# Kernel tuning notes

Measured on AMD Instinct MI355X. Metric: run time of the kernel, lower is better.

The kernel has to match this reference:

```python
import jax, jax.numpy as jnp
import numpy as np

N = 50000       # nodes
E = 800000      # edges (before self-loops)
F_IN = 128
HID = 64
HEADS = 4
OUT_DIM = 128
N_CLS = 2
NG = 500        # num graphs
SLOPE = 0.2     # GATConv leaky_relu negative slope
EPS = 1e-5      # BatchNorm eps


def setup_inputs() -> dict:
    key = jax.random.key(0)
    ks = jax.random.split(key, 24)
    s = 0.05
    d = {
        "x": jax.random.normal(ks[0], (N, F_IN), jnp.float32),
        "edge_index": jax.random.randint(ks[1], (2, E), 0, N, jnp.int64),
        "batch": jnp.sort(jax.random.randint(ks[2], (N,), 0, NG, jnp.int64)),
        # GATConv 1
        "W1": jax.random.normal(ks[3], (F_IN, HEADS * HID), jnp.float32) * s,
        "att_src1": jax.random.normal(ks[4], (HEADS, HID), jnp.float32) * s,
        "att_dst1": jax.random.normal(ks[5], (HEADS, HID), jnp.float32) * s,
        "b1": jnp.zeros((HEADS * HID,), jnp.float32),
        # BN1 (eval mode)
        "g1": jnp.ones((HEADS * HID,), jnp.float32),
        "be1": jnp.zeros((HEADS * HID,), jnp.float32),
        "rm1": jnp.zeros((HEADS * HID,), jnp.float32),
        "rv1": jnp.ones((HEADS * HID,), jnp.float32),
        # GATConv 2
        "W2": jax.random.normal(ks[6], (HEADS * HID, HEADS * HID), jnp.float32) * s,
        "att_src2": jax.random.normal(ks[7], (HEADS, HID), jnp.float32) * s,
        "att_dst2": jax.random.normal(ks[8], (HEADS, HID), jnp.float32) * s,
        "b2": jnp.zeros((HEADS * HID,), jnp.float32),
        # BN2 (eval mode)
        "g2": jnp.ones((HEADS * HID,), jnp.float32),
        "be2": jnp.zeros((HEADS * HID,), jnp.float32),
        "rm2": jnp.zeros((HEADS * HID,), jnp.float32),
        "rv2": jnp.ones((HEADS * HID,), jnp.float32),
        # MLP head
        "lw1": jax.random.normal(ks[9], (HEADS * HID, OUT_DIM), jnp.float32) * s,
        "lb1": jnp.zeros((OUT_DIM,), jnp.float32),
        "lw2": jax.random.normal(ks[10], (OUT_DIM, N_CLS), jnp.float32) * s,
        "lb2": jnp.zeros((N_CLS,), jnp.float32),
    }
    return d


def _gat_conv(x, src, dst, W, a_src, a_dst, b):
    """PyG GATConv (concat heads, add_self_loops=True, eval -> no dropout)."""
    n = x.shape[0]
    h = (x @ W).reshape(n, HEADS, -1)            # [N, H, C]
    loop = jnp.arange(n)
    s = jnp.concatenate([src, loop])             # self-loops appended
    d = jnp.concatenate([dst, loop])
    a_s = jnp.sum(h * a_src, axis=-1)            # [N, H]
    a_d = jnp.sum(h * a_dst, axis=-1)            # [N, H]
    e = jax.nn.leaky_relu(a_s[s] + a_d[d], SLOPE)   # [Et, H]
    # softmax over incoming edges per destination node
    m = jax.ops.segment_max(e, d, num_segments=n)
    ex = jnp.exp(e - m[d])
    denom = jax.ops.segment_sum(ex, d, num_segments=n)
    alpha = ex / denom[d]                        # [Et, H]
    msg = h[s] * alpha[:, :, None]               # [Et, H, C]
    out = jax.ops.segment_sum(msg, d, num_segments=n)
    return out.reshape(n, -1) + b


def _bn_eval(x, g, be, rm, rv):
    return (x - rm) * jax.lax.rsqrt(rv + EPS) * g + be


def reference(x, edge_index, batch, W1, att_src1, att_dst1, b1, g1, be1, rm1, rv1,
              W2, att_src2, att_dst2, b2, g2, be2, rm2, rv2, lw1, lb1, lw2, lb2):
    src, dst = edge_index[0], edge_index[1]
    h = jax.nn.relu(_gat_conv(x, src, dst, W1, att_src1, att_dst1, b1))
    h = _bn_eval(h, g1, be1, rm1, rv1)
    h = jax.nn.relu(_gat_conv(h, src, dst, W2, att_src2, att_dst2, b2))
    h = _bn_eval(h, g2, be2, rm2, rv2)
    # global mean pool over graphs
    sums = jax.ops.segment_sum(h, batch, num_segments=NG)
    cnt = jax.ops.segment_sum(jnp.ones((h.shape[0],), h.dtype), batch, num_segments=NG)
    pooled = sums / jnp.clip(cnt, 1.0)[:, None]
    z = jax.nn.relu(pooled @ lw1 + lb1)
    return z @ lw2 + lb2
```

## Files before the change

### kernel.cpp

```cpp
#include <hip/hip_runtime.h>
#include <hip/hip_bf16.h>
#include <math.h>

#define N_NODES 50000
#define M_PAD   50048
#define TILE_M  64
#define NBLK_GEMM (M_PAD / TILE_M)
#define N_EDGES 800000
#define EHALF   (N_EDGES / 2)
#define NBLK_BUILD ((EHALF + 255) / 256)
#define F_IN 128
#define HID 64
#define HEADS 4
#define FEAT 256
#define OUT_DIM 128
#define N_CLS 2
#define NG 500
#define SLOPE 0.2f
#define BN_EPS 1e-5f
#define ECAP 64

#define XCONV (N_NODES * F_IN / 8)
#define T_W1  (F_IN * 256)
#define T_W2  (FEAT * 256)
#define XPAD_ULL ((M_PAD - N_NODES) * F_IN / 4)
#define HPAD_ULL ((M_PAD - N_NODES) * FEAT / 4)
#define PREP_THREADS (XCONV + T_W1 + T_W2 + XPAD_ULL + HPAD_ULL + N_NODES)
#define NBLK_PREP ((PREP_THREADS + 255) / 256)

typedef __attribute__((ext_vector_type(8))) short short8;
typedef __attribute__((ext_vector_type(4))) float floatx4;
typedef __attribute__((ext_vector_type(2))) float floatx2;

__device__ inline unsigned short f2bf(float f) {
    unsigned int u = __float_as_uint(f);
    unsigned int lsb = (u >> 16) & 1u;
    return (unsigned short)((u + 0x7fffu + lsb) >> 16);
}

__global__ __launch_bounds__(256) void prep(
    const float* __restrict__ x, const float* __restrict__ W1,
    const float* __restrict__ W2,
    unsigned short* __restrict__ xbf, unsigned short* __restrict__ W1T,
    unsigned short* __restrict__ W2T, unsigned short* __restrict__ h1bf,
    int* __restrict__ deg, unsigned short* __restrict__ ell,
    int* __restrict__ ovf_cnt) {
    int gid = blockIdx.x * 256 + threadIdx.x;
    if (gid < XCONV) {
        const float4* xp = (const float4*)&x[gid * 8];
        float4 f0 = xp[0], f1 = xp[1];
        uint4 pk;
        pk.x = (unsigned)f2bf(f0.x) | ((unsigned)f2bf(f0.y) << 16);
        pk.y = (unsigned)f2bf(f0.z) | ((unsigned)f2bf(f0.w) << 16);
        pk.z = (unsigned)f2bf(f1.x) | ((unsigned)f2bf(f1.y) << 16);
        pk.w = (unsigned)f2bf(f1.z) | ((unsigned)f2bf(f1.w) << 16);
        *(uint4*)&xbf[gid * 8] = pk;
        return;
    }
    int j = gid - XCONV;
    if (j < T_W1) {
        int k = j >> 8, n = j & 255;
        W1T[n * F_IN + k] = f2bf(W1[j]);
        return;
    }
    j -= T_W1;
    if (j < T_W2) {
        int k = j >> 8, n = j & 255;
        W2T[n * FEAT + k] = f2bf(W2[j]);
        return;
    }
    j -= T_W2;
    if (j < XPAD_ULL) {
        ((unsigned long long*)(xbf + (size_t)N_NODES * F_IN))[j] = 0ULL;
        return;
    }
    j -= XPAD_ULL;
    if (j < HPAD_ULL) {
        ((unsigned long long*)(h1bf + (size_t)N_NODES * FEAT))[j] = 0ULL;
        return;
    }
    j -= HPAD_ULL;
    if (j < N_NODES) {
        deg[j] = 1;
        ell[(size_t)j * ECAP] = (unsigned short)j;
        if (j == 0) *ovf_cnt = 0;
    }
}

template<int K, bool BUILD>
__global__ __launch_bounds__(256, 4) void gemm_mfma(
    const unsigned short* __restrict__ Ab, const unsigned short* __restrict__ BT,
    const float* __restrict__ att_src, const float* __restrict__ att_dst,
    unsigned char* __restrict__ h8, float* __restrict__ a_s,
    float* __restrict__ a_d,
    const int* __restrict__ src, const int* __restrict__ dst,
    int* __restrict__ deg, unsigned short* __restrict__ ell,
    int* __restrict__ ovf_cnt, int* __restrict__ ovf) {
    constexpr int LS = 40;
    constexpr int C8 = 272;
    __shared__ __align__(16) unsigned char smem_raw[(TILE_M + FEAT) * LS * 2];
    int t = threadIdx.x;

    if (BUILD && blockIdx.x < NBLK_BUILD) {
        int i = blockIdx.x * 256 + t;
        if (i >= EHALF) return;
        int s0 = src[i],          d0 = dst[i];
        int s1 = src[i + EHALF],  d1 = dst[i + EHALF];
        int p0 = atomicAdd(&deg[d0], 1);
        int p1 = atomicAdd(&deg[d1], 1);
        if (p0 < ECAP) {
            ell[(size_t)d0 * ECAP + p0] = (unsigned short)s0;
        } else {
            int k = atomicAdd(ovf_cnt, 1);
            ovf[2 * k] = s0; ovf[2 * k + 1] = d0;
        }
        if (p1 < ECAP) {
            ell[(size_t)d1 * ECAP + p1] = (unsigned short)s1;
        } else {
            int k = atomicAdd(ovf_cnt, 1);
            ovf[2 * k] = s1; ovf[2 * k + 1] = d1;
        }
        return;
    }

    int bid = BUILD ? (int)blockIdx.x - NBLK_BUILD : (int)blockIdx.x;
    unsigned short* As = (unsigned short*)smem_raw;
    unsigned short* Bs = As + TILE_M * LS;
    unsigned char*  s8 = smem_raw;
    int lane = t & 63, w = t >> 6;
    int row0 = bid * TILE_M;
    int mrow = lane & 15, quad = lane >> 4;

    floatx4 acc[4][4] = {};

    int rA = t >> 2, cA = (t & 3) * 8;

    for (int k0 = 0; k0 < K; k0 += 32) {
        *(uint4*)&As[rA * LS + cA] =
            *(const uint4*)&Ab[(long long)(row0 + rA) * K + k0 + cA];
        #pragma unroll
        for (int j = 0; j < 4; j++) {
            int r = rA + j * 64;
            *(uint4*)&Bs[r * LS + cA] = *(const uint4*)&BT[(long long)r * K + k0 + cA];
        }
        __syncthreads();
        short8 bf[4];
        #pragma unroll
        for (int ni = 0; ni < 4; ni++)
            bf[ni] = *(const short8*)&Bs[(w * 64 + ni * 16 + mrow) * LS + quad * 8];
        #pragma unroll
        for (int mi = 0; mi < 4; mi++) {
            short8 af = *(const short8*)&As[(mi * 16 + mrow) * LS + quad * 8];
            #pragma unroll
            for (int ni = 0; ni < 4; ni++)
                acc[mi][ni] = __builtin_amdgcn_mfma_f32_16x16x32_bf16(af, bf[ni],
                                                                      acc[mi][ni], 0, 0, 0);
        }
        __syncthreads();
    }

    float ats[4], atd[4];
    #pragma unroll
    for (int ni = 0; ni < 4; ni++) {
        ats[ni] = att_src[w * 64 + ni * 16 + mrow];
        atd[ni] = att_dst[w * 64 + ni * 16 + mrow];
    }
    #pragma unroll
    for (int mi = 0; mi < 4; mi++) {
        #pragma unroll
        for (int r = 0; r < 4; r++) {
            int row = row0 + mi * 16 + quad * 4 + r;
            float ps = 0.f, pd = 0.f;
            #pragma unroll
            for (int ni = 0; ni < 4; ni++) {
                float v = acc[mi][ni][r];
                ps += v * ats[ni];
                pd += v * atd[ni];
            }
            #pragma unroll
            for (int off = 1; off < 16; off <<= 1) {
                ps += __shfl_xor(ps, off);
                pd += __shfl_xor(pd, off);
            }
            if (mrow == 0 && row < N_NODES) {
                a_s[row * 4 + w] = ps;
                a_d[row * 4 + w] = pd;
            }
        }
    }

    #pragma unroll
    for (int mi = 0; mi < 4; mi++)
        #pragma unroll
        for (int r = 0; r < 4; r++) {
            int row = mi * 16 + quad * 4 + r;
            #pragma unroll
            for (int ni = 0; ni < 4; ni += 2) {
                int pk = __builtin_amdgcn_cvt_pk_fp8_f32(acc[mi][ni][r],
                                                         acc[mi][ni + 1][r], 0, false);
                s8[row * C8 + w * 64 + ni * 16 + mrow]       = (unsigned char)(pk & 0xff);
                s8[row * C8 + w * 64 + (ni + 1) * 16 + mrow] = (unsigned char)((pk >> 8) & 0xff);
            }
        }
    __syncthreads();
    {
        int r2 = t >> 2, q = t & 3;
        const uint4* sp = (const uint4*)&s8[r2 * C8 + q * 64];
        uint4* dp = (uint4*)&h8[(long long)(row0 + r2) * FEAT + q * 64];
        #pragma unroll
        for (int k = 0; k < 4; k++)
            dp[k] = sp[k];
    }
}

__global__ __launch_bounds__(256) void gat_fused(
    const int* __restrict__ deg_arr, const unsigned short* __restrict__ ell,
    const int* __restrict__ ovf_cnt, const int* __restrict__ ovf,
    const float* __restrict__ a_s, const float* __restrict__ a_d,
    const unsigned char* __restrict__ h8, const float* __restrict__ bias,
    const float* __restrict__ g, const float* __restrict__ be,
    const float* __restrict__ rm, const float* __restrict__ rv,
    unsigned short* __restrict__ out16) {
    int t = threadIdx.x;
    int lane = t & 63;
    int w = t >> 6;
    int hd = lane >> 4;
    int d = blockIdx.x * 4 + w;

    __shared__ float p_lds[4 * ECAP * 4];
    __shared__ int   o_lds[4 * ECAP];
    float* pw = &p_lds[w * ECAP * 4];
    int*   ow = &o_lds[w * ECAP];

    const unsigned int* __restrict__ H1 = (const unsigned int*)h8;

    int deg = deg_arr[d];
    float4 ad4 = *(const float4*)&a_d[d * 4];

    float den = 0.f;
    float4 acc = make_float4(0.f, 0.f, 0.f, 0.f);

    if (deg <= ECAP) {
        float lg[4] = {-INFINITY, -INFINITY, -INFINITY, -INFINITY};
        if (lane < deg) {
            int s = ell[(size_t)d * ECAP + lane];
            ow[lane] = s * 64;
            float4 as4 = *(const float4*)&a_s[s * 4];
            float e0 = as4.x + ad4.x; lg[0] = e0 > 0.f ? e0 : SLOPE * e0;
            float e1 = as4.y + ad4.y; lg[1] = e1 > 0.f ? e1 : SLOPE * e1;
            float e2 = as4.z + ad4.z; lg[2] = e2 > 0.f ? e2 : SLOPE * e2;
            float e3 = as4.w + ad4.w; lg[3] = e3 > 0.f ? e3 : SLOPE * e3;
        }
        float mm = fmaxf(fmaxf(lg[0], lg[1]), fmaxf(lg[2], lg[3]));
        #pragma unroll
        for (int off = 1; off < 64; off <<= 1) mm = fmaxf(mm, __shfl_xor(mm, off));
        if (lane < deg) {
            float4 pq;
            pq.x = __expf(lg[0] - mm);
            pq.y = __expf(lg[1] - mm);
            pq.z = __expf(lg[2] - mm);
            pq.w = __expf(lg[3] - mm);
            *(float4*)&pw[lane * 4] = pq;
        }
        int e = 0;
        for (; e + 1 < deg; e += 2) {
            int oA = ow[e], oB = ow[e + 1];
            float pA = pw[e * 4 + hd], pB = pw[(e + 1) * 4 + hd];
            int uA = (int)H1[oA + lane];
            int uB = (int)H1[oB + lane];
            den += pA + pB;
            floatx2 a0 = __builtin_amdgcn_cvt_pk_f32_fp8(uA, false);
            floatx2 a1 = __builtin_amdgcn_cvt_pk_f32_fp8(uA, true);
            floatx2 b0 = __builtin_amdgcn_cvt_pk_f32_fp8(uB, false);
            floatx2 b1 = __builtin_amdgcn_cvt_pk_f32_fp8(uB, true);
            acc.x += pA * a0.x; acc.y += pA * a0.y;
            acc.z += pA * a1.x; acc.w += pA * a1.y;
            acc.x += pB * b0.x; acc.y += pB * b0.y;
            acc.z += pB * b1.x; acc.w += pB * b1.y;
        }
        if (e < deg) {
            int oA = ow[e];
            float pA = pw[e * 4 + hd];
            int uA = (int)H1[oA + lane];
            den += pA;
            floatx2 a0 = __builtin_amdgcn_cvt_pk_f32_fp8(uA, false);
            floatx2 a1 = __builtin_amdgcn_cvt_pk_f32_fp8(uA, true);
            acc.x += pA * a0.x; acc.y += pA * a0.y;
            acc.z += pA * a1.x; acc.w += pA * a1.y;
        }
    } else {
        float m_old;
        {
            int s = ell[(size_t)d * ECAP + lane];
            ow[lane] = s * 64;
            float4 as4 = *(const float4*)&a_s[s * 4];
            float lg[4];
            float e0 = as4.x + ad4.x; lg[0] = e0 > 0.f ? e0 : SLOPE * e0;
            float e1 = as4.y + ad4.y; lg[1] = e1 > 0.f ? e1 : SLOPE * e1;
            float e2 = as4.z + ad4.z; lg[2] = e2 > 0.f ? e2 : SLOPE * e2;
            float e3 = as4.w + ad4.w; lg[3] = e3 > 0.f ? e3 : SLOPE * e3;
            float mm = fmaxf(fmaxf(lg[0], lg[1]), fmaxf(lg[2], lg[3]));
            #pragma unroll
            for (int off = 1; off < 64; off <<= 1) mm = fmaxf(mm, __shfl_xor(mm, off));
            m_old = mm;
            float4 pq;
            pq.x = __expf(lg[0] - mm);
            pq.y = __expf(lg[1] - mm);
            pq.z = __expf(lg[2] - mm);
            pq.w = __expf(lg[3] - mm);
            *(float4*)&pw[lane * 4] = pq;
            for (int e = 0; e < ECAP; e++) {
                int oA = ow[e];
                float pA = pw[e * 4 + hd];
                int uA = (int)H1[oA + lane];
                den += pA;
                floatx2 a0 = __builtin_amdgcn_cvt_pk_f32_fp8(uA, false);
                floatx2 a1 = __builtin_amdgcn_cvt_pk_f32_fp8(uA, true);
                acc.x += pA * a0.x; acc.y += pA * a0.y;
                acc.z += pA * a1.x; acc.w += pA * a1.y;
            }
        }
        int nov = *ovf_cnt;
        for (int i = 0; i < nov; i++) {
            int s2 = ovf[2 * i], d2 = ovf[2 * i + 1];
            if (d2 != d) continue;
            float4 as4 = *(const float4*)&a_s[s2 * 4];
            float lg[4];
            float e0 = as4.x + ad4.x; lg[0] = e0 > 0.f ? e0 : SLOPE * e0;
            float e1 = as4.y + ad4.y; lg[1] = e1 > 0.f ? e1 : SLOPE * e1;
            float e2 = as4.z + ad4.z; lg[2] = e2 > 0.f ? e2 : SLOPE * e2;
            float e3 = as4.w + ad4.w; lg[3] = e3 > 0.f ? e3 : SLOPE * e3;
            float mmax = fmaxf(fmaxf(lg[0], lg[1]), fmaxf(lg[2], lg[3]));
            float m_new = fmaxf(m_old, mmax);
            float alpha = __expf(m_old - m_new);
            m_old = m_new;
            float ph = __expf(lg[hd] - m_new);
            acc.x *= alpha; acc.y *= alpha; acc.z *= alpha; acc.w *= alpha;
            den = den * alpha + ph;
            int u = (int)H1[s2 * 64 + lane];
            floatx2 a0 = __builtin_amdgcn_cvt_pk_f32_fp8(u, false);
            floatx2 a1 = __builtin_amdgcn_cvt_pk_f32_fp8(u, true);
            acc.x += ph * a0.x; acc.y += ph * a0.y;
            acc.z += ph * a1.x; acc.w += ph * a1.y;
        }
    }
    float inv = 1.f / den;
    int c0 = lane * 4;
    float4 bi = *(const float4*)&bias[c0];
    float4 gg = *(const float4*)&g[c0];
    float4 bb = *(const float4*)&be[c0];
    float4 mm4 = *(const float4*)&rm[c0];
    float4 vv = *(const float4*)&rv[c0];
    float v0 = fmaxf(acc.x * inv + bi.x, 0.f);
    float v1 = fmaxf(acc.y * inv + bi.y, 0.f);
    float v2 = fmaxf(acc.z * inv + bi.z, 0.f);
    float v3 = fmaxf(acc.w * inv + bi.w, 0.f);
    v0 = (v0 - mm4.x) * rsqrtf(vv.x + BN_EPS) * gg.x + bb.x;
    v1 = (v1 - mm4.y) * rsqrtf(vv.y + BN_EPS) * gg.y + bb.y;
    v2 = (v2 - mm4.z) * rsqrtf(vv.z + BN_EPS) * gg.z + bb.z;
    v3 = (v3 - mm4.w) * rsqrtf(vv.w + BN_EPS) * gg.w + bb.w;
    unsigned long long o =
        (unsigned long long)f2bf(v0) |
        ((unsigned long long)f2bf(v1) << 16) |
        ((unsigned long long)f2bf(v2) << 32) |
        ((unsigned long long)f2bf(v3) << 48);
    __builtin_nontemporal_store(o, (unsigned long long*)&out16[(long long)d * FEAT + c0]);
}

__global__ __launch_bounds__(256) void head_fused(
    const unsigned short* __restrict__ h2, const int* __restrict__ batch,
    const float* __restrict__ lw1, const float* __restrict__ lb1,
    const float* __restrict__ lw2, const float* __restrict__ lb2,
    float* __restrict__ out) {
    int gph = blockIdx.x;
    int t = threadIdx.x;
    __shared__ float pooled[FEAT];
    __shared__ float zl[OUT_DIM];
    __shared__ int lo_s, hi_s;
    if (t == 0) {
        int lo = 0, hi = N_NODES;
        while (lo < hi) { int mid = (lo + hi) >> 1; if (batch[mid] < gph) lo = mid + 1; else hi = mid; }
        lo_s = lo;
        int lo2 = 0, hi2 = N_NODES;
        while (lo2 < hi2) { int mid = (lo2 + hi2) >> 1; if (batch[mid] < gph + 1) lo2 = mid + 1; else hi2 = mid; }
        hi_s = lo2;
    }
    __syncthreads();
    int lo = lo_s, hi = hi_s;
    float a0 = 0.f, a1 = 0.f, a2 = 0.f, a3 = 0.f;
    int n = lo;
    for (; n + 3 < hi; n += 4) {
        a0 += __uint_as_float((unsigned)h2[(long long)n * FEAT + t] << 16);
        a1 += __uint_as_float((unsigned)h2[(long long)(n + 1) * FEAT + t] << 16);
        a2 += __uint_as_float((unsigned)h2[(long long)(n + 2) * FEAT + t] << 16);
        a3 += __uint_as_float((unsigned)h2[(long long)(n + 3) * FEAT + t] << 16);
    }
    for (; n < hi; n++) a0 += __uint_as_float((unsigned)h2[(long long)n * FEAT + t] << 16);
    float cnt = fmaxf((float)(hi - lo), 1.f);
    pooled[t] = (a0 + a1 + a2 + a3) / cnt;
    __syncthreads();
    int j = t >> 1, kh = t & 1;
    float zp = 0.f;
    #pragma unroll 8
    for (int k = kh * 128; k < kh * 128 + 128; k++)
        zp += pooled[k] * lw1[k * OUT_DIM + j];
    zp += __shfl_xor(zp, 1);
    if (kh == 0) zl[j] = fmaxf(zp + lb1[j], 0.f);
    __syncthreads();
    int w = t >> 6, lane = t & 63;
    if (w < 2) {
        float p = zl[lane] * lw2[lane * 2 + w] + zl[lane + 64] * lw2[(lane + 64) * 2 + w];
        #pragma unroll
        for (int off = 1; off < 64; off <<= 1) p += __shfl_xor(p, off);
        if (lane == 0) out[gph * 2 + w] = p + lb2[w];
    }
}

extern "C" void kernel_launch(void* const* d_in, const int* in_sizes, int n_in,
                              void* d_out, int out_size, void* d_ws, size_t ws_size,
                              hipStream_t stream) {
    const float* x       = (const float*)d_in[0];
    const int*   ei      = (const int*)d_in[1];
    const int*   batch   = (const int*)d_in[2];
    const float* W1      = (const float*)d_in[3];
    const float* att_s1  = (const float*)d_in[4];
    const float* att_d1  = (const float*)d_in[5];
    const float* b1      = (const float*)d_in[6];
    const float* g1      = (const float*)d_in[7];
    const float* be1     = (const float*)d_in[8];
    const float* rm1     = (const float*)d_in[9];
    const float* rv1     = (const float*)d_in[10];
    const float* W2      = (const float*)d_in[11];
    const float* att_s2  = (const float*)d_in[12];
    const float* att_d2  = (const float*)d_in[13];
    const float* b2      = (const float*)d_in[14];
    const float* g2      = (const float*)d_in[15];
    const float* be2     = (const float*)d_in[16];
    const float* rm2     = (const float*)d_in[17];
    const float* rv2     = (const float*)d_in[18];
    const float* lw1     = (const float*)d_in[19];
    const float* lb1     = (const float*)d_in[20];
    const float* lw2     = (const float*)d_in[21];
    const float* lb2     = (const float*)d_in[22];
    float* out           = (float*)d_out;

    const int* src = ei;
    const int* dst = ei + N_EDGES;

    char* p = (char*)d_ws;
    auto carve = [&p](size_t bytes) -> void* {
        void* r = (void*)p;
        p += (bytes + 63) & ~(size_t)63;
        return r;
    };
    unsigned short* h2bf = (unsigned short*)carve(sizeof(short) * (size_t)N_NODES * FEAT);
    float* a_s    = (float*)carve(sizeof(float) * N_NODES * HEADS);
    float* a_d    = (float*)carve(sizeof(float) * N_NODES * HEADS);
    int*   deg    = (int*)carve(sizeof(int) * N_NODES);
    int*   ovf_cnt= (int*)carve(sizeof(int) * 16);
    unsigned short* ell = (unsigned short*)carve(sizeof(short) * (size_t)N_NODES * ECAP);
    int*   ovf    = (int*)carve(sizeof(int) * 2 * (N_EDGES + N_NODES));
    unsigned char*  h8   = (unsigned char*)carve((size_t)M_PAD * FEAT);
    unsigned short* xbf  = (unsigned short*)carve(sizeof(short) * (size_t)M_PAD * F_IN);
    unsigned short* h1bf = (unsigned short*)carve(sizeof(short) * (size_t)M_PAD * FEAT);
    unsigned short* w1t  = (unsigned short*)carve(sizeof(short) * FEAT * F_IN);
    unsigned short* w2t  = (unsigned short*)carve(sizeof(short) * FEAT * FEAT);

    prep<<<NBLK_PREP, 256, 0, stream>>>(
        x, W1, W2, xbf, w1t, w2t, h1bf, deg, ell, ovf_cnt);

    gemm_mfma<F_IN, true><<<NBLK_BUILD + NBLK_GEMM, 256, 0, stream>>>(
        xbf, w1t, att_s1, att_d1, h8, a_s, a_d,
        src, dst, deg, ell, ovf_cnt, ovf);
    gat_fused<<<N_NODES / 4, 256, 0, stream>>>(deg, ell, ovf_cnt, ovf, a_s, a_d, h8,
                                               b1, g1, be1, rm1, rv1, h1bf);

    gemm_mfma<FEAT, false><<<NBLK_GEMM, 256, 0, stream>>>(
        h1bf, w2t, att_s2, att_d2, h8, a_s, a_d,
        nullptr, nullptr, nullptr, nullptr, nullptr, nullptr);
    gat_fused<<<N_NODES / 4, 256, 0, stream>>>(deg, ell, ovf_cnt, ovf, a_s, a_d, h8,
                                               b2, g2, be2, rm2, rv2, h2bf);

    head_fused<<<NG, 256, 0, stream>>>(h2bf, batch, lw1, lb1, lw2, lb2, out);
}
```

Before: 309.9 us.

## Fuse x bf16 conversion into GEMM1 and software-pipeline GAT neighbor gathers

Drops the separate x-to-bf16 conversion pass in prep and converts fp32 x to bf16 while loading the A tile inside the first GEMM, which saves a full write and reread of the converted input. GEMM blocks are now placed before the edge-build blocks in the combined launch. The GAT aggregation loop is rewritten to gather four neighbor rows per step, with the next group prefetched (zero-padded to a multiple of four), so more loads are in flight. The ELL neighbor list widens from 16-bit to 32-bit indices, which doubles its memory traffic.

```diff
diff --git a/kernel.cpp b/kernel.cpp
--- a/kernel.cpp
+++ b/kernel.cpp
@@ -20,12 +20,10 @@
 #define BN_EPS 1e-5f
 #define ECAP 64
 
-#define XCONV (N_NODES * F_IN / 8)
 #define T_W1  (F_IN * 256)
 #define T_W2  (FEAT * 256)
-#define XPAD_ULL ((M_PAD - N_NODES) * F_IN / 4)
 #define HPAD_ULL ((M_PAD - N_NODES) * FEAT / 4)
-#define PREP_THREADS (XCONV + T_W1 + T_W2 + XPAD_ULL + HPAD_ULL + N_NODES)
+#define PREP_THREADS (T_W1 + T_W2 + HPAD_ULL + N_NODES)
 #define NBLK_PREP ((PREP_THREADS + 255) / 256)
 
 typedef __attribute__((ext_vector_type(8))) short short8;
@@ -38,43 +36,24 @@
     return (unsigned short)((u + 0x7fffu + lsb) >> 16);
 }
 
-__global__ __launch_bounds__(256) void prep(
-    const float* __restrict__ x, const float* __restrict__ W1,
-    const float* __restrict__ W2,
-    unsigned short* __restrict__ xbf, unsigned short* __restrict__ W1T,
-    unsigned short* __restrict__ W2T, unsigned short* __restrict__ h1bf,
-    int* __restrict__ deg, unsigned short* __restrict__ ell,
-    int* __restrict__ ovf_cnt) {
+__global__ __launch_bounds__(256) void prep_small(
+    const float* __restrict__ W1, const float* __restrict__ W2,
+    unsigned short* __restrict__ W1T, unsigned short* __restrict__ W2T,
+    unsigned short* __restrict__ h1bf,
+    int* __restrict__ deg, int* __restrict__ ell, int* __restrict__ ovf_cnt) {
     int gid = blockIdx.x * 256 + threadIdx.x;
-    if (gid < XCONV) {
-        const float4* xp = (const float4*)&x[gid * 8];
-        float4 f0 = xp[0], f1 = xp[1];
-        uint4 pk;
-        pk.x = (unsigned)f2bf(f0.x) | ((unsigned)f2bf(f0.y) << 16);
-        pk.y = (unsigned)f2bf(f0.z) | ((unsigned)f2bf(f0.w) << 16);
-        pk.z = (unsigned)f2bf(f1.x) | ((unsigned)f2bf(f1.y) << 16);
-        pk.w = (unsigned)f2bf(f1.z) | ((unsigned)f2bf(f1.w) << 16);
-        *(uint4*)&xbf[gid * 8] = pk;
+    if (gid < T_W1) {
+        int k = gid >> 8, n = gid & 255;
+        W1T[n * F_IN + k] = f2bf(W1[gid]);
         return;
     }
-    int j = gid - XCONV;
-    if (j < T_W1) {
-        int k = j >> 8, n = j & 255;
-        W1T[n * F_IN + k] = f2bf(W1[j]);
-        return;
-    }
-    j -= T_W1;
+    int j = gid - T_W1;
     if (j < T_W2) {
         int k = j >> 8, n = j & 255;
         W2T[n * FEAT + k] = f2bf(W2[j]);
         return;
     }
     j -= T_W2;
-    if (j < XPAD_ULL) {
-        ((unsigned long long*)(xbf + (size_t)N_NODES * F_IN))[j] = 0ULL;
-        return;
-    }
-    j -= XPAD_ULL;
     if (j < HPAD_ULL) {
         ((unsigned long long*)(h1bf + (size_t)N_NODES * FEAT))[j] = 0ULL;
         return;
@@ -82,139 +61,171 @@
     j -= HPAD_ULL;
     if (j < N_NODES) {
         deg[j] = 1;
-        ell[(size_t)j * ECAP] = (unsigned short)j;
+        ell[(size_t)j * ECAP] = j;
         if (j == 0) *ovf_cnt = 0;
     }
 }
 
-template<int K, bool BUILD>
-__global__ __launch_bounds__(256, 4) void gemm_mfma(
-    const unsigned short* __restrict__ Ab, const unsigned short* __restrict__ BT,
+template<int K, bool AF32>
+__device__ __forceinline__ void gemm_core(
+    const void* __restrict__ Av, const unsigned short* __restrict__ BT,
+    const float* __restrict__ att_src, const float* __restrict__ att_dst,
+    unsigned char* __restrict__ h8, float* __restrict__ a_s,
+    float* __restrict__ a_d, int bid, unsigned char* smem_raw) {
+    constexpr int LS = 40;
+    constexpr int C8 = 272;
+    int t = threadIdx.x;
+    unsigned short* As = (unsigned short*)smem_raw;
+    unsigned short* Bs = As + TILE_M * LS;
+    unsigned char*  s8 = smem_raw;
+    int lane = t & 63, w = t >> 6;
+    int row0 = bid * TILE_M;
+    int mrow = lane & 15, quad = lane >> 4;
+
+    floatx4 acc[4][4] = {};
+
+    int rA = t >> 2, cA = (t & 3) * 8;
+
+    const unsigned short* Ab = (const unsigned short*)Av;
+    const float* Af = (const float*)Av;
+
+    for (int k0 = 0; k0 < K; k0 += 32) {
+        if (AF32) {
+            uint4 pk = make_uint4(0, 0, 0, 0);
+            if (row0 + rA < N_NODES) {
+                float4 f0 = *(const float4*)&Af[(long long)(row0 + rA) * K + k0 + cA];
+                float4 f1 = *(const float4*)&Af[(long long)(row0 + rA) * K + k0 + cA + 4];
+                pk.x = (unsigned)f2bf(f0.x) | ((unsigned)f2bf(f0.y) << 16);
+                pk.y = (unsigned)f2bf(f0.z) | ((unsigned)f2bf(f0.w) << 16);
+                pk.z = (unsigned)f2bf(f1.x) | ((unsigned)f2bf(f1.y) << 16);
+                pk.w = (unsigned)f2bf(f1.z) | ((unsigned)f2bf(f1.w) << 16);
+            }
+            *(uint4*)&As[rA * LS + cA] = pk;
+        } else {
+            *(uint4*)&As[rA * LS + cA] =
+                *(const uint4*)&Ab[(long long)(row0 + rA) * K + k0 + cA];
+        }
+        #pragma unroll
+        for (int j = 0; j < 4; j++) {
+            int r = rA + j * 64;
+            *(uint4*)&Bs[r * LS + cA] = *(const uint4*)&BT[(long long)r * K + k0 + cA];
+        }
+        __syncthreads();
+        short8 bf[4];
+        #pragma unroll
+        for (int ni = 0; ni < 4; ni++)
+            bf[ni] = *(const short8*)&Bs[(w * 64 + ni * 16 + mrow) * LS + quad * 8];
+        #pragma unroll
+        for (int mi = 0; mi < 4; mi++) {
+            short8 af = *(const short8*)&As[(mi * 16 + mrow) * LS + quad * 8];
+            #pragma unroll
+            for (int ni = 0; ni < 4; ni++)
+                acc[mi][ni] = __builtin_amdgcn_mfma_f32_16x16x32_bf16(af, bf[ni],
+                                                                      acc[mi][ni], 0, 0, 0);
+        }
+        __syncthreads();
+    }
+
+    float ats[4], atd[4];
+    #pragma unroll
+    for (int ni = 0; ni < 4; ni++) {
+        ats[ni] = att_src[w * 64 + ni * 16 + mrow];
+        atd[ni] = att_dst[w * 64 + ni * 16 + mrow];
+    }
+    #pragma unroll
+    for (int mi = 0; mi < 4; mi++) {
+        #pragma unroll
+        for (int r = 0; r < 4; r++) {
+            int row = row0 + mi * 16 + quad * 4 + r;
+            float ps = 0.f, pd = 0.f;
+            #pragma unroll
+            for (int ni = 0; ni < 4; ni++) {
+                float v = acc[mi][ni][r];
+                ps += v * ats[ni];
+                pd += v * atd[ni];
+            }
+            #pragma unroll
+            for (int off = 1; off < 16; off <<= 1) {
+                ps += __shfl_xor(ps, off);
+                pd += __shfl_xor(pd, off);
+            }
+            if (mrow == 0 && row < N_NODES) {
+                a_s[row * 4 + w] = ps;
+                a_d[row * 4 + w] = pd;
+            }
+        }
+    }
+
+    #pragma unroll
+    for (int mi = 0; mi < 4; mi++)
+        #pragma unroll
+        for (int r = 0; r < 4; r++) {
+            int row = mi * 16 + quad * 4 + r;
+            #pragma unroll
+            for (int ni = 0; ni < 4; ni += 2) {
+                int pk = __builtin_amdgcn_cvt_pk_fp8_f32(acc[mi][ni][r],
+                                                         acc[mi][ni + 1][r], 0, false);
+                s8[row * C8 + w * 64 + ni * 16 + mrow]       = (unsigned char)(pk & 0xff);
+                s8[row * C8 + w * 64 + (ni + 1) * 16 + mrow] = (unsigned char)((pk >> 8) & 0xff);
+            }
+        }
+    __syncthreads();
+    {
+        int r2 = t >> 2, q = t & 3;
+        const uint4* sp = (const uint4*)&s8[r2 * C8 + q * 64];
+        uint4* dp = (uint4*)&h8[(long long)(row0 + r2) * FEAT + q * 64];
+        #pragma unroll
+        for (int k = 0; k < 4; k++)
+            dp[k] = sp[k];
+    }
+}
+
+__global__ __launch_bounds__(256, 4) void gemm1_build(
+    const float* __restrict__ x, const unsigned short* __restrict__ BT,
     const float* __restrict__ att_src, const float* __restrict__ att_dst,
     unsigned char* __restrict__ h8, float* __restrict__ a_s,
     float* __restrict__ a_d,
     const int* __restrict__ src, const int* __restrict__ dst,
-    int* __restrict__ deg, unsigned short* __restrict__ ell,
+    int* __restrict__ deg, int* __restrict__ ell,
     int* __restrict__ ovf_cnt, int* __restrict__ ovf) {
-    constexpr int LS = 40;
-    constexpr int C8 = 272;
-    __shared__ __align__(16) unsigned char smem_raw[(TILE_M + FEAT) * LS * 2];
-    int t = threadIdx.x;
-
-    if (BUILD && blockIdx.x < NBLK_BUILD) {
-        int i = blockIdx.x * 256 + t;
+    __shared__ __align__(16) unsigned char smem_raw[(TILE_M + FEAT) * 40 * 2];
+    if (blockIdx.x >= NBLK_GEMM) {
+        int i = (blockIdx.x - NBLK_GEMM) * 256 + threadIdx.x;
         if (i >= EHALF) return;
         int s0 = src[i],          d0 = dst[i];
         int s1 = src[i + EHALF],  d1 = dst[i + EHALF];
         int p0 = atomicAdd(&deg[d0], 1);
         int p1 = atomicAdd(&deg[d1], 1);
         if (p0 < ECAP) {
-            ell[(size_t)d0 * ECAP + p0] = (unsigned short)s0;
+            ell[(size_t)d0 * ECAP + p0] = s0;
         } else {
             int k = atomicAdd(ovf_cnt, 1);
             ovf[2 * k] = s0; ovf[2 * k + 1] = d0;
         }
         if (p1 < ECAP) {
-            ell[(size_t)d1 * ECAP + p1] = (unsigned short)s1;
+            ell[(size_t)d1 * ECAP + p1] = s1;
         } else {
             int k = atomicAdd(ovf_cnt, 1);
             ovf[2 * k] = s1; ovf[2 * k + 1] = d1;
         }
         return;
     }
-
-    int bid = BUILD ? (int)blockIdx.x - NBLK_BUILD : (int)blockIdx.x;
-    unsigned short* As = (unsigned short*)smem_raw;
-    unsigned short* Bs = As + TILE_M * LS;
-    unsigned char*  s8 = smem_raw;
-    int lane = t & 63, w = t >> 6;
-    int row0 = bid * TILE_M;
-    int mrow = lane & 15, quad = lane >> 4;
-
-    floatx4 acc[4][4] = {};
-
-    int rA = t >> 2, cA = (t & 3) * 8;
-
-    for (int k0 = 0; k0 < K; k0 += 32) {
-        *(uint4*)&As[rA * LS + cA] =
-            *(const uint4*)&Ab[(long long)(row0 + rA) * K + k0 + cA];
-        #pragma unroll
-        for (int j = 0; j < 4; j++) {
-            int r = rA + j * 64;
-            *(uint4*)&Bs[r * LS + cA] = *(const uint4*)&BT[(long long)r * K + k0 + cA];
-        }
-        __syncthreads();
-        short8 bf[4];
-        #pragma unroll
-        for (int ni = 0; ni < 4; ni++)
-            bf[ni] = *(const short8*)&Bs[(w * 64 + ni * 16 + mrow) * LS + quad * 8];
-        #pragma unroll
-        for (int mi = 0; mi < 4; mi++) {
-            short8 af = *(const short8*)&As[(mi * 16 + mrow) * LS + quad * 8];
-            #pragma unroll
-            for (int ni = 0; ni < 4; ni++)
-                acc[mi][ni] = __builtin_amdgcn_mfma_f32_16x16x32_bf16(af, bf[ni],
-                                                                      acc[mi][ni], 0, 0, 0);
-        }
-        __syncthreads();
-    }
-
-    float ats[4], atd[4];
-    #pragma unroll
-    for (int ni = 0; ni < 4; ni++) {
-        ats[ni] = att_src[w * 64 + ni * 16 + mrow];
-        atd[ni] = att_dst[w * 64 + ni * 16 + mrow];
-    }
-    #pragma unroll
-    for (int mi = 0; mi < 4; mi++) {
-        #pragma unroll
-        for (int r = 0; r < 4; r++) {
-            int row = row0 + mi * 16 + quad * 4 + r;
-            float ps = 0.f, pd = 0.f;
-            #pragma unroll
-            for (int ni = 0; ni < 4; ni++) {
-                float v = acc[mi][ni][r];
-                ps += v * ats[ni];
-                pd += v * atd[ni];
-            }
-            #pragma unroll
-            for (int off = 1; off < 16; off <<= 1) {
-                ps += __shfl_xor(ps, off);
-                pd += __shfl_xor(pd, off);
-            }
-            if (mrow == 0 && row < N_NODES) {
-                a_s[row * 4 + w] = ps;
-                a_d[row * 4 + w] = pd;
-            }
-        }
-    }
-
-    #pragma unroll
-    for (int mi = 0; mi < 4; mi++)
-        #pragma unroll
-        for (int r = 0; r < 4; r++) {
-            int row = mi * 16 + quad * 4 + r;
-            #pragma unroll
-            for (int ni = 0; ni < 4; ni += 2) {
-                int pk = __builtin_amdgcn_cvt_pk_fp8_f32(acc[mi][ni][r],
-                                                         acc[mi][ni + 1][r], 0, false);
-                s8[row * C8 + w * 64 + ni * 16 + mrow]       = (unsigned char)(pk & 0xff);
-                s8[row * C8 + w * 64 + (ni + 1) * 16 + mrow] = (unsigned char)((pk >> 8) & 0xff);
-            }
-        }
-    __syncthreads();
-    {
-        int r2 = t >> 2, q = t & 3;
-        const uint4* sp = (const uint4*)&s8[r2 * C8 + q * 64];
-        uint4* dp = (uint4*)&h8[(long long)(row0 + r2) * FEAT + q * 64];
-        #pragma unroll
-        for (int k = 0; k < 4; k++)
-            dp[k] = sp[k];
-    }
-}
-
-__global__ __launch_bounds__(256) void gat_fused(
-    const int* __restrict__ deg_arr, const unsigned short* __restrict__ ell,
+    gemm_core<F_IN, true>(x, BT, att_src, att_dst, h8, a_s, a_d,
+                          blockIdx.x, smem_raw);
+}
+
+__global__ __launch_bounds__(256, 4) void gemm2k(
+    const unsigned short* __restrict__ Ab, const unsigned short* __restrict__ BT,
+    const float* __restrict__ att_src, const float* __restrict__ att_dst,
+    unsigned char* __restrict__ h8, float* __restrict__ a_s,
+    float* __restrict__ a_d) {
+    __shared__ __align__(16) unsigned char smem_raw[(TILE_M + FEAT) * 40 * 2];
+    gemm_core<FEAT, false>(Ab, BT, att_src, att_dst, h8, a_s, a_d,
+                           blockIdx.x, smem_raw);
+}
+
+__device__ __forceinline__ void gat_core(
+    const int* __restrict__ deg_arr, const int* __restrict__ ell,
     const int* __restrict__ ovf_cnt, const int* __restrict__ ovf,
     const float* __restrict__ a_s, const float* __restrict__ a_d,
     const unsigned char* __restrict__ h8, const float* __restrict__ bias,
@@ -242,51 +253,48 @@
 
     if (deg <= ECAP) {
         float lg[4] = {-INFINITY, -INFINITY, -INFINITY, -INFINITY};
+        int s = 0;
         if (lane < deg) {
-            int s = ell[(size_t)d * ECAP + lane];
-            ow[lane] = s * 64;
+            s = ell[(size_t)d * ECAP + lane];
             float4 as4 = *(const float4*)&a_s[s * 4];
             float e0 = as4.x + ad4.x; lg[0] = e0 > 0.f ? e0 : SLOPE * e0;
             float e1 = as4.y + ad4.y; lg[1] = e1 > 0.f ? e1 : SLOPE * e1;
             float e2 = as4.z + ad4.z; lg[2] = e2 > 0.f ? e2 : SLOPE * e2;
             float e3 = as4.w + ad4.w; lg[3] = e3 > 0.f ? e3 : SLOPE * e3;
         }
+        ow[lane] = s * 64;
         float mm = fmaxf(fmaxf(lg[0], lg[1]), fmaxf(lg[2], lg[3]));
         #pragma unroll
         for (int off = 1; off < 64; off <<= 1) mm = fmaxf(mm, __shfl_xor(mm, off));
+        float4 pq = make_float4(0.f, 0.f, 0.f, 0.f);
         if (lane < deg) {
-            float4 pq;
             pq.x = __expf(lg[0] - mm);
             pq.y = __expf(lg[1] - mm);
             pq.z = __expf(lg[2] - mm);
             pq.w = __expf(lg[3] - mm);
-            *(float4*)&pw[lane * 4] = pq;
-        }
-        int e = 0;
-        for (; e + 1 < deg; e += 2) {
-            int oA = ow[e], oB = ow[e + 1];
-            float pA = pw[e * 4 + hd], pB = pw[(e + 1) * 4 + hd];
-            int uA = (int)H1[oA + lane];
-            int uB = (int)H1[oB + lane];
-            den += pA + pB;
-            floatx2 a0 = __builtin_amdgcn_cvt_pk_f32_fp8(uA, false);
-            floatx2 a1 = __builtin_amdgcn_cvt_pk_f32_fp8(uA, true);
-            floatx2 b0 = __builtin_amdgcn_cvt_pk_f32_fp8(uB, false);
-            floatx2 b1 = __builtin_amdgcn_cvt_pk_f32_fp8(uB, true);
-            acc.x += pA * a0.x; acc.y += pA * a0.y;
-            acc.z += pA * a1.x; acc.w += pA * a1.y;
-            acc.x += pB * b0.x; acc.y += pB * b0.y;
-            acc.z += pB * b1.x; acc.w += pB * b1.y;
-        }
-        if (e < deg) {
-            int oA = ow[e];
-            float pA = pw[e * 4 + hd];
-            int uA = (int)H1[oA + lane];
-            den += pA;
-            floatx2 a0 = __builtin_amdgcn_cvt_pk_f32_fp8(uA, false);
-            floatx2 a1 = __builtin_amdgcn_cvt_pk_f32_fp8(uA, true);
-            acc.x += pA * a0.x; acc.y += pA * a0.y;
-            acc.z += pA * a1.x; acc.w += pA * a1.y;
+        }
+        *(float4*)&pw[lane * 4] = pq;
+        int deg4 = (deg + 3) & ~3;
+        int cu[4];
+        #pragma unroll
+        for (int j = 0; j < 4; j++) cu[j] = (int)H1[ow[j] + lane];
+        for (int e = 0; e < deg4; e += 4) {
+            int nu[4] = {0, 0, 0, 0};
+            if (e + 4 < deg4) {
+                #pragma unroll
+                for (int j = 0; j < 4; j++) nu[j] = (int)H1[ow[e + 4 + j] + lane];
+            }
+            #pragma unroll
+            for (int j = 0; j < 4; j++) {
+                float pj = pw[(e + j) * 4 + hd];
+                den += pj;
+                floatx2 lo = __builtin_amdgcn_cvt_pk_f32_fp8(cu[j], false);
+                floatx2 hi = __builtin_amdgcn_cvt_pk_f32_fp8(cu[j], true);
+                acc.x += pj * lo.x; acc.y += pj * lo.y;
+                acc.z += pj * hi.x; acc.w += pj * hi.y;
+            }
+            #pragma unroll
+            for (int j = 0; j < 4; j++) cu[j] = nu[j];
         }
     } else {
         float m_old;
@@ -365,6 +373,28 @@
         ((unsigned long long)f2bf(v2) << 32) |
         ((unsigned long long)f2bf(v3) << 48);
     __builtin_nontemporal_store(o, (unsigned long long*)&out16[(long long)d * FEAT + c0]);
+}
+
+__global__ __launch_bounds__(256) void gat1(
+    const int* __restrict__ deg_arr, const int* __restrict__ ell,
+    const int* __restrict__ ovf_cnt, const int* __restrict__ ovf,
+    const float* __restrict__ a_s, const float* __restrict__ a_d,
+    const unsigned char* __restrict__ h8, const float* __restrict__ bias,
+    const float* __restrict__ g, const float* __restrict__ be,
+    const float* __restrict__ rm, const float* __restrict__ rv,
+    unsigned short* __restrict__ out16) {
+    gat_core(deg_arr, ell, ovf_cnt, ovf, a_s, a_d, h8, bias, g, be, rm, rv, out16);
+}
+
+__global__ __launch_bounds__(256) void gat2(
+    const int* __restrict__ deg_arr, const int* __restrict__ ell,
+    const int* __restrict__ ovf_cnt, const int* __restrict__ ovf,
+    const float* __restrict__ a_s, const float* __restrict__ a_d,
+    const unsigned char* __restrict__ h8, const float* __restrict__ bias,
+    const float* __restrict__ g, const float* __restrict__ be,
+    const float* __restrict__ rm, const float* __restrict__ rv,
+    unsigned short* __restrict__ out16) {
+    gat_core(deg_arr, ell, ovf_cnt, ovf, a_s, a_d, h8, bias, g, be, rm, rv, out16);
 }
 
 __global__ __launch_bounds__(256) void head_fused(
@@ -458,28 +488,26 @@
     float* a_d    = (float*)carve(sizeof(float) * N_NODES * HEADS);
     int*   deg    = (int*)carve(sizeof(int) * N_NODES);
     int*   ovf_cnt= (int*)carve(sizeof(int) * 16);
-    unsigned short* ell = (unsigned short*)carve(sizeof(short) * (size_t)N_NODES * ECAP);
+    int*   ell    = (int*)carve(sizeof(int) * (size_t)N_NODES * ECAP);
     int*   ovf    = (int*)carve(sizeof(int) * 2 * (N_EDGES + N_NODES));
     unsigned char*  h8   = (unsigned char*)carve((size_t)M_PAD * FEAT);
-    unsigned short* xbf  = (unsigned short*)carve(sizeof(short) * (size_t)M_PAD * F_IN);
     unsigned short* h1bf = (unsigned short*)carve(sizeof(short) * (size_t)M_PAD * FEAT);
     unsigned short* w1t  = (unsigned short*)carve(sizeof(short) * FEAT * F_IN);
     unsigned short* w2t  = (unsigned short*)carve(sizeof(short) * FEAT * FEAT);
 
-    prep<<<NBLK_PREP, 256, 0, stream>>>(
-        x, W1, W2, xbf, w1t, w2t, h1bf, deg, ell, ovf_cnt);
-
-    gemm_mfma<F_IN, true><<<NBLK_BUILD + NBLK_GEMM, 256, 0, stream>>>(
-        xbf, w1t, att_s1, att_d1, h8, a_s, a_d,
+    prep_small<<<NBLK_PREP, 256, 0, stream>>>(
+        W1, W2, w1t, w2t, h1bf, deg, ell, ovf_cnt);
+
+    gemm1_build<<<NBLK_GEMM + NBLK_BUILD, 256, 0, stream>>>(
+        x, w1t, att_s1, att_d1, h8, a_s, a_d,
         src, dst, deg, ell, ovf_cnt, ovf);
-    gat_fused<<<N_NODES / 4, 256, 0, stream>>>(deg, ell, ovf_cnt, ovf, a_s, a_d, h8,
-                                               b1, g1, be1, rm1, rv1, h1bf);
-
-    gemm_mfma<FEAT, false><<<NBLK_GEMM, 256, 0, stream>>>(
-        h1bf, w2t, att_s2, att_d2, h8, a_s, a_d,
-        nullptr, nullptr, nullptr, nullptr, nullptr, nullptr);
-    gat_fused<<<N_NODES / 4, 256, 0, stream>>>(deg, ell, ovf_cnt, ovf, a_s, a_d, h8,
-                                               b2, g2, be2, rm2, rv2, h2bf);
+    gat1<<<N_NODES / 4, 256, 0, stream>>>(deg, ell, ovf_cnt, ovf, a_s, a_d, h8,
+                                          b1, g1, be1, rm1, rv1, h1bf);
+
+    gemm2k<<<NBLK_GEMM, 256, 0, stream>>>(
+        h1bf, w2t, att_s2, att_d2, h8, a_s, a_d);
+    gat2<<<N_NODES / 4, 256, 0, stream>>>(deg, ell, ovf_cnt, ovf, a_s, a_d, h8,
+                                          b2, g2, be2, rm2, rv2, h2bf);
 
     head_fused<<<NG, 256, 0, stream>>>(h2bf, batch, lw1, lb1, lw2, lb2, out);
 }
```

Measured after the change: 300.1 us. -3.2%, faster.
